# Kernel tuning notes

Hardware: AMD Instinct MI355X
Metric: run time of the kernel (lower is better)

The kernel has to match this reference:

```python
import jax, jax.numpy as jnp
import numpy as np

B = 8
N1, N2 = 65536, 16384
C1, C2 = 256, 512
BN_EPS = 1e-5


def setup_inputs() -> dict:
    key = jax.random.key(0)
    ks = jax.random.split(key, 8)
    xyz1 = jax.random.normal(ks[0], (N1, 3), dtype=jnp.float32)
    points1 = jax.random.normal(ks[1], (N1, C1), dtype=jnp.float32)
    xyz2 = jax.random.normal(ks[2], (N2, 3), dtype=jnp.float32)
    points2 = jax.random.normal(ks[3], (N2, C2), dtype=jnp.float32)
    offset1 = (jnp.arange(1, B + 1, dtype=jnp.int32) * (N1 // B))
    offset2 = (jnp.arange(1, B + 1, dtype=jnp.int32) * (N2 // B))
    W1 = jax.random.normal(ks[4], (C1 + C2, 256), dtype=jnp.float32) * 0.02
    b1 = jnp.zeros((256,), jnp.float32)
    g1 = jnp.ones((256,), jnp.float32)
    be1 = jnp.zeros((256,), jnp.float32)
    W2 = jax.random.normal(ks[5], (256, 256), dtype=jnp.float32) * 0.02
    b2 = jnp.zeros((256,), jnp.float32)
    g2 = jnp.ones((256,), jnp.float32)
    be2 = jnp.zeros((256,), jnp.float32)
    return dict(xyz1=xyz1, points1=points1, xyz2=xyz2, points2=points2,
                offset1=offset1, offset2=offset2,
                W1=W1, b1=b1, g1=g1, be1=be1, W2=W2, b2=b2, g2=g2, be2=be2)


def _knn3(q, k):
    # q: [n1,3] queries, k: [n2,3] reference set -> 3-NN idx + euclidean dist
    d2 = (jnp.sum(q * q, -1)[:, None] + jnp.sum(k * k, -1)[None, :]
          - 2.0 * (q @ k.T))                      # [n1, n2]
    neg_d2, idx = jax.lax.top_k(-d2, 3)           # [n1, 3]
    dist = jnp.sqrt(jnp.maximum(-neg_d2, 0.0))
    return idx, dist


def _bn_relu(x, g, be):
    # BatchNorm1d in training mode: biased batch stats over the point dim
    mu = jnp.mean(x, axis=0)
    var = jnp.mean((x - mu) ** 2, axis=0)
    return jax.nn.relu(g * (x - mu) * jax.lax.rsqrt(var + BN_EPS) + be)


def reference(xyz1, points1, xyz2, points2, offset1, offset2,
              W1, b1, g1, be1, W2, b2, g2, be2):
    bsz = offset1.shape[0]
    n1 = xyz1.shape[0] // bsz
    n2 = xyz2.shape[0] // bsz
    q = xyz1.reshape(bsz, n1, 3)
    k = xyz2.reshape(bsz, n2, 3)
    idx, dist = jax.vmap(_knn3)(q, k)             # [B,n1,3], [B,n1,3]
    gidx = (idx + (jnp.arange(bsz, dtype=idx.dtype) * n2)[:, None, None])
    gidx = gidx.reshape(-1, 3)                    # [N1,3] global row ids
    dist = dist.reshape(-1, 3)
    dist_recip = 1.0 / (dist + 1e-8)
    weight = dist_recip / jnp.sum(dist_recip, axis=1, keepdims=True)
    # fused gather + weighted accumulate: [N1,3,C2] * [N1,3,1] -> [N1,C2]
    interpolated = jnp.sum(points2[gidx] * weight[..., None], axis=1)
    x = jnp.concatenate([points1, interpolated], axis=1)  # [N1, C1+C2]
    x = _bn_relu(x @ W1 + b1, g1, be1)
    x = _bn_relu(x @ W2 + b2, g2, be2)
    return x
```

## Files before the change

### kernel.cpp

```cpp
#include <hip/hip_runtime.h>
#include <math.h>

#define N1T 65536
#define N2T 16384
#define BSZ 8
#define N1B 8192
#define N2B 2048
#define C1 256
#define C2 512
#define K1 768
#define HID 256
#define BN_EPS 1e-5f

typedef short bf16x8 __attribute__((ext_vector_type(8)));
typedef float f32x4 __attribute__((ext_vector_type(4)));

__device__ __forceinline__ float mul_rn(float a, float b) {
    float r; asm("v_mul_f32 %0, %1, %2" : "=v"(r) : "v"(a), "v"(b)); return r;
}
__device__ __forceinline__ float add_rn(float a, float b) {
    float r; asm("v_add_f32 %0, %1, %2" : "=v"(r) : "v"(a), "v"(b)); return r;
}
__device__ __forceinline__ float sub_rn(float a, float b) {
    float r; asm("v_sub_f32 %0, %1, %2" : "=v"(r) : "v"(a), "v"(b)); return r;
}
__device__ __forceinline__ float fma_rn(float a, float b, float c) {
    float r; asm("v_fma_f32 %0, %1, %2, %3" : "=v"(r) : "v"(a), "v"(b), "v"(c)); return r;
}
__device__ __forceinline__ short f2bf(float f) {
    unsigned u = __builtin_bit_cast(unsigned, f);
    u += 0x7fffu + ((u >> 16) & 1u);
    return (short)(u >> 16);
}
__device__ __forceinline__ float bf2f(short s) {
    return __builtin_bit_cast(float, ((unsigned)(unsigned short)s) << 16);
}

__global__ __launch_bounds__(256) void knn_kernel(
    const float* __restrict__ xyz1, const float* __restrict__ xyz2,
    int* __restrict__ idx_out, float* __restrict__ w_out)
{
    __shared__ float4 sref[N2B + 4];
    const int tid = threadIdx.x;
    const int qbase = blockIdx.x * 64;
    const int batch = qbase / N1B;
    const float* k2 = xyz2 + (size_t)batch * N2B * 3;
    for (int p = tid; p < N2B; p += 256) {
        float x = k2[3 * p], y = k2[3 * p + 1], z = k2[3 * p + 2];
        float kk = add_rn(add_rn(mul_rn(x, x), mul_rn(y, y)), mul_rn(z, z));
        sref[p + (p >> 9)] = make_float4(x, y, z, kk);
    }
    __syncthreads();

    const int q = qbase + (tid >> 2);
    const int sub = tid & 3;
    const float qx = xyz1[q * 3 + 0], qy = xyz1[q * 3 + 1], qz = xyz1[q * 3 + 2];
    const float qq = add_rn(add_rn(mul_rn(qx, qx), mul_rn(qy, qy)), mul_rn(qz, qz));

    const int base = sub * 513;
    const int gbase = sub * 512;
    float a0 = 1e30f, a1 = 1e30f, a2 = 1e30f;
    int   ai0 = 0x7fffffff, ai1 = 0x7fffffff, ai2 = 0x7fffffff;
    float c0 = 1e30f, c1 = 1e30f, c2 = 1e30f;
    int   ci0 = 0x7fffffff, ci1 = 0x7fffffff, ci2 = 0x7fffffff;
    for (int jj = 0; jj < 256; ++jj) {
        float4 rA = sref[base + jj];
        float4 rB = sref[base + 256 + jj];
        float pA = mul_rn(qx, rA.x);
        float tA = fma_rn(qz, rA.z, fma_rn(qy, rA.y, pA));
        float dA = add_rn(sub_rn(qq, add_rn(tA, tA)), rA.w);
        float pB = mul_rn(qx, rB.x);
        float tB = fma_rn(qz, rB.z, fma_rn(qy, rB.y, pB));
        float dB = add_rn(sub_rn(qq, add_rn(tB, tB)), rB.w);
        if (dA < a2) {
            if (dA < a1) {
                a2 = a1; ai2 = ai1;
                if (dA < a0) { a1 = a0; ai1 = ai0; a0 = dA; ai0 = gbase + jj; }
                else         { a1 = dA; ai1 = gbase + jj; }
            } else { a2 = dA; ai2 = gbase + jj; }
        }
        if (dB < c2) {
            if (dB < c1) {
                c2 = c1; ci2 = ci1;
                if (dB < c0) { c1 = c0; ci1 = ci0; c0 = dB; ci0 = gbase + 256 + jj; }
                else         { c1 = dB; ci1 = gbase + 256 + jj; }
            } else { c2 = dB; ci2 = gbase + 256 + jj; }
        }
    }
    float bd0 = a0, bd1 = a1, bd2 = a2;
    int   bi0 = ai0, bi1 = ai1, bi2 = ai2;
#define LEXINS(d, ji)                                                        \
    if ((d < bd2) || (d == bd2 && ji < bi2)) {                               \
        if ((d < bd1) || (d == bd1 && ji < bi1)) {                           \
            bd2 = bd1; bi2 = bi1;                                            \
            if ((d < bd0) || (d == bd0 && ji < bi0)) {                       \
                bd1 = bd0; bi1 = bi0; bd0 = d; bi0 = ji;                     \
            } else { bd1 = d; bi1 = ji; }                                    \
        } else { bd2 = d; bi2 = ji; }                                        \
    }
    LEXINS(c0, ci0) LEXINS(c1, ci1) LEXINS(c2, ci2)
#pragma unroll
    for (int mask = 1; mask <= 2; mask <<= 1) {
        float pd0 = __shfl_xor(bd0, mask, 64);
        float pd1 = __shfl_xor(bd1, mask, 64);
        float pd2 = __shfl_xor(bd2, mask, 64);
        int   pi0 = __shfl_xor(bi0, mask, 64);
        int   pi1 = __shfl_xor(bi1, mask, 64);
        int   pi2 = __shfl_xor(bi2, mask, 64);
        LEXINS(pd0, pi0) LEXINS(pd1, pi1) LEXINS(pd2, pi2)
    }
#undef LEXINS
    if (sub == 0) {
        float d0s = __fsqrt_rn(fmaxf(bd0, 0.0f));
        float d1s = __fsqrt_rn(fmaxf(bd1, 0.0f));
        float d2s = __fsqrt_rn(fmaxf(bd2, 0.0f));
        float r0 = __fdiv_rn(1.0f, add_rn(d0s, 1e-8f));
        float r1 = __fdiv_rn(1.0f, add_rn(d1s, 1e-8f));
        float r2 = __fdiv_rn(1.0f, add_rn(d2s, 1e-8f));
        float rs = add_rn(add_rn(r0, r1), r2);
        w_out[q * 3 + 0] = __fdiv_rn(r0, rs);
        w_out[q * 3 + 1] = __fdiv_rn(r1, rs);
        w_out[q * 3 + 2] = __fdiv_rn(r2, rs);
        idx_out[q * 3 + 0] = batch * N2B + bi0;
        idx_out[q * 3 + 1] = batch * N2B + bi1;
        idx_out[q * 3 + 2] = batch * N2B + bi2;
    }
}

__global__ __launch_bounds__(256) void cast_p2_kernel(
    const float* __restrict__ p2, short* __restrict__ p2b)
{
    const size_t i = ((size_t)blockIdx.x * 256 + threadIdx.x) * 8;
    float4 u0 = *(const float4*)(p2 + i);
    float4 u1 = *(const float4*)(p2 + i + 4);
    bf16x8 v;
    v[0] = f2bf(u0.x); v[1] = f2bf(u0.y); v[2] = f2bf(u0.z); v[3] = f2bf(u0.w);
    v[4] = f2bf(u1.x); v[5] = f2bf(u1.y); v[6] = f2bf(u1.z); v[7] = f2bf(u1.w);
    *(bf16x8*)(p2b + i) = v;
}

__global__ __launch_bounds__(256) void transpose_w1_kernel(
    const float* __restrict__ W1, short* __restrict__ w1at, short* __restrict__ w1bt)
{
    const int e = blockIdx.x * 256 + threadIdx.x;
    const int k = e / HID, n = e % HID;
    short v = f2bf(W1[e]);
    if (k < C1) w1at[(size_t)n * C1 + k] = v;
    else        w1bt[(size_t)n * C2 + (k - C1)] = v;
}

__global__ __launch_bounds__(256) void transpose_w_kernel(
    const float* __restrict__ Win, short* __restrict__ WT, int K, int N)
{
    const int e = blockIdx.x * 256 + threadIdx.x;
    const int k = e / N, n = e % N;
    WT[(size_t)n * K + k] = f2bf(Win[e]);
}

#define LDP 40

__global__ __launch_bounds__(256) void zgemm_kernel(
    const short* __restrict__ p2b, const short* __restrict__ w1bt,
    float* __restrict__ Z)
{
    __shared__ short As[128][LDP];
    __shared__ short Bs[128][LDP];
    const int tid = threadIdx.x;
    const int lane = tid & 63, wv = tid >> 6;
    const int wr = wv >> 1, wc = wv & 1;
    const int l16 = lane & 15, kh = (lane >> 4) * 8;
    const int row0 = blockIdx.y * 128, col0 = blockIdx.x * 128;
    f32x4 acc[4][4];
#pragma unroll
    for (int m = 0; m < 4; ++m)
#pragma unroll
        for (int n = 0; n < 4; ++n) acc[m][n] = (f32x4){0.f, 0.f, 0.f, 0.f};

    const int c0 = tid * 2;
    const int r0c = c0 >> 2, kc0 = (c0 & 3) * 8;
    const int r1c = (c0 + 1) >> 2, kc1 = ((c0 + 1) & 3) * 8;

    for (int kt = 0; kt < C2 / 32; ++kt) {
        const int k0 = kt * 32;
        bf16x8 va = *(const bf16x8*)(p2b + (size_t)(row0 + r0c) * C2 + k0 + kc0);
        bf16x8 vb = *(const bf16x8*)(p2b + (size_t)(row0 + r1c) * C2 + k0 + kc1);
        bf16x8 wa = *(const bf16x8*)(w1bt + (size_t)(col0 + r0c) * C2 + k0 + kc0);
        bf16x8 wb = *(const bf16x8*)(w1bt + (size_t)(col0 + r1c) * C2 + k0 + kc1);
        __syncthreads();
        *(bf16x8*)(&As[r0c][kc0]) = va;
        *(bf16x8*)(&As[r1c][kc1]) = vb;
        *(bf16x8*)(&Bs[r0c][kc0]) = wa;
        *(bf16x8*)(&Bs[r1c][kc1]) = wb;
        __syncthreads();

        bf16x8 af[4], bf[4];
#pragma unroll
        for (int m = 0; m < 4; ++m)
            af[m] = *(const bf16x8*)(&As[wr * 64 + m * 16 + l16][kh]);
#pragma unroll
        for (int n = 0; n < 4; ++n)
            bf[n] = *(const bf16x8*)(&Bs[wc * 64 + n * 16 + l16][kh]);
#pragma unroll
        for (int m = 0; m < 4; ++m)
#pragma unroll
            for (int n = 0; n < 4; ++n)
                acc[m][n] = __builtin_amdgcn_mfma_f32_16x16x32_bf16(
                    af[m], bf[n], acc[m][n], 0, 0, 0);
    }
#pragma unroll
    for (int n = 0; n < 4; ++n) {
        const int col = col0 + wc * 64 + n * 16 + l16;
#pragma unroll
        for (int m = 0; m < 4; ++m) {
            const int rowb = row0 + wr * 64 + m * 16 + (lane >> 4) * 4;
#pragma unroll
            for (int j = 0; j < 4; ++j)
                Z[(size_t)(rowb + j) * HID + col] = acc[m][n][j];
        }
    }
}

__global__ __launch_bounds__(512) void gemm1m_kernel(
    const float* __restrict__ points1, const float* __restrict__ Z,
    const int* __restrict__ idx, const float* __restrict__ w,
    const short* __restrict__ w1at, const float* __restrict__ bias,
    short* __restrict__ y1b, float* __restrict__ psum, float* __restrict__ psq)
{
    __shared__ short As[128][LDP];
    __shared__ short Bs[256][LDP];
    __shared__ int   sidx[128][3];
    __shared__ float swt[128][3];
    __shared__ float redS[2][4][64], redQ[2][4][64];
    const int tid = threadIdx.x;
    const int lane = tid & 63, wv = tid >> 6;
    const int wr = wv >> 2, wc = wv & 3;
    const int l16 = lane & 15, kh = (lane >> 4) * 8;
    const int row0 = blockIdx.x * 128;

    if (tid < 128) {
        sidx[tid][0] = idx[(row0 + tid) * 3 + 0];
        sidx[tid][1] = idx[(row0 + tid) * 3 + 1];
        sidx[tid][2] = idx[(row0 + tid) * 3 + 2];
        swt[tid][0] = w[(row0 + tid) * 3 + 0];
        swt[tid][1] = w[(row0 + tid) * 3 + 1];
        swt[tid][2] = w[(row0 + tid) * 3 + 2];
    }

    f32x4 acc[4][4];
#pragma unroll
    for (int m = 0; m < 4; ++m)
#pragma unroll
        for (int n = 0; n < 4; ++n) acc[m][n] = (f32x4){0.f, 0.f, 0.f, 0.f};

    const int arow = tid >> 2, akc = (tid & 3) * 8;
    const int rowA = row0 + arow;
    const int cb0 = tid * 2, cb1 = tid * 2 + 1;
    const int brow0 = cb0 >> 2, bkc0 = (cb0 & 3) * 8;
    const int brow1 = cb1 >> 2, bkc1 = (cb1 & 3) * 8;

#define LOAD_A(VA, KT)                                                        \
    {                                                                         \
        const int k0_ = (KT) * 32;                                            \
        float4 u0 = *(const float4*)(points1 + (size_t)rowA * C1 + k0_ + akc);     \
        float4 u1 = *(const float4*)(points1 + (size_t)rowA * C1 + k0_ + akc + 4); \
        VA[0] = f2bf(u0.x); VA[1] = f2bf(u0.y); VA[2] = f2bf(u0.z); VA[3] = f2bf(u0.w); \
        VA[4] = f2bf(u1.x); VA[5] = f2bf(u1.y); VA[6] = f2bf(u1.z); VA[7] = f2bf(u1.w); \
    }
#define LOAD_B(WA, WB, KT)                                                    \
    {                                                                         \
        const int k0_ = (KT) * 32;                                            \
        WA = *(const bf16x8*)(w1at + (size_t)brow0 * C1 + k0_ + bkc0);        \
        WB = *(const bf16x8*)(w1at + (size_t)brow1 * C1 + k0_ + bkc1);        \
    }

    bf16x8 va, wa, wb;
    LOAD_A(va, 0)
    LOAD_B(wa, wb, 0)
    for (int kt = 0; kt < C1 / 32; ++kt) {
        __syncthreads();
        *(bf16x8*)(&As[arow][akc]) = va;
        *(bf16x8*)(&Bs[brow0][bkc0]) = wa;
        *(bf16x8*)(&Bs[brow1][bkc1]) = wb;
        __syncthreads();
        if (kt + 1 < C1 / 32) {
            LOAD_A(va, kt + 1)
            LOAD_B(wa, wb, kt + 1)
        }
        bf16x8 af[4], bf[4];
#pragma unroll
        for (int m = 0; m < 4; ++m)
            af[m] = *(const bf16x8*)(&As[wr * 64 + m * 16 + l16][kh]);
#pragma unroll
        for (int n = 0; n < 4; ++n)
            bf[n] = *(const bf16x8*)(&Bs[wc * 64 + n * 16 + l16][kh]);
#pragma unroll
        for (int m = 0; m < 4; ++m)
#pragma unroll
            for (int n = 0; n < 4; ++n)
                acc[m][n] = __builtin_amdgcn_mfma_f32_16x16x32_bf16(
                    af[m], bf[n], acc[m][n], 0, 0, 0);
    }
#undef LOAD_A
#undef LOAD_B
    float bv[4];
#pragma unroll
    for (int n = 0; n < 4; ++n) bv[n] = bias[wc * 64 + n * 16 + l16];
    float s[4] = {0.f, 0.f, 0.f, 0.f}, qa[4] = {0.f, 0.f, 0.f, 0.f};
#pragma unroll
    for (int m = 0; m < 4; ++m) {
        const int rl0 = wr * 64 + m * 16 + (lane >> 4) * 4;
#pragma unroll
        for (int j = 0; j < 4; ++j) {
            const int rl = rl0 + j;
            const int j0 = sidx[rl][0], j1 = sidx[rl][1], j2 = sidx[rl][2];
            const float w0 = swt[rl][0], w1 = swt[rl][1], w2 = swt[rl][2];
            const float* z0 = Z + (size_t)j0 * HID;
            const float* z1 = Z + (size_t)j1 * HID;
            const float* z2 = Z + (size_t)j2 * HID;
#pragma unroll
            for (int n = 0; n < 4; ++n) {
                const int col = wc * 64 + n * 16 + l16;
                float zi = fmaf(w0, z0[col], fmaf(w1, z1[col], w2 * z2[col]));
                float v = acc[m][n][j] + bv[n] + zi;
                y1b[(size_t)(row0 + rl) * HID + col] = f2bf(v);
                s[n] += v; qa[n] = fmaf(v, v, qa[n]);
            }
        }
    }
#pragma unroll
    for (int n = 0; n < 4; ++n) {
        float sv = s[n], qv = qa[n];
        sv += __shfl_xor(sv, 16, 64);  sv += __shfl_xor(sv, 32, 64);
        qv += __shfl_xor(qv, 16, 64);  qv += __shfl_xor(qv, 32, 64);
        if ((lane >> 4) == 0) {
            redS[wr][wc][n * 16 + l16] = sv;
            redQ[wr][wc][n * 16 + l16] = qv;
        }
    }
    __syncthreads();
    if (tid < 256) {
        const int wcf = tid >> 6, cf = tid & 63;
        float sv = redS[0][wcf][cf] + redS[1][wcf][cf];
        float qv = redQ[0][wcf][cf] + redQ[1][wcf][cf];
        psum[(size_t)blockIdx.x * HID + tid] = sv;
        psq[(size_t)blockIdx.x * HID + tid] = qv;
    }
}

#define GEMM_EPILOGUE(STORE_STMT)                                             \
    __shared__ float redS[2][2][64], redQ[2][2][64];                          \
    _Pragma("unroll")                                                         \
    for (int n = 0; n < 4; ++n) {                                             \
        const int col = col0 + wc * 64 + n * 16 + l16;                        \
        const float bv = bias[col];                                           \
        float s = 0.f, qa = 0.f;                                              \
        _Pragma("unroll")                                                     \
        for (int m = 0; m < 4; ++m) {                                         \
            const int rowb = row0 + wr * 64 + m * 16 + (lane >> 4) * 4;       \
            _Pragma("unroll")                                                 \
            for (int j = 0; j < 4; ++j) {                                     \
                float v = acc[m][n][j] + bv;                                  \
                STORE_STMT;                                                   \
                s += v; qa = fmaf(v, v, qa);                                  \
            }                                                                 \
        }                                                                     \
        s += __shfl_xor(s, 16, 64);  s += __shfl_xor(s, 32, 64);              \
        qa += __shfl_xor(qa, 16, 64); qa += __shfl_xor(qa, 32, 64);           \
        if ((lane >> 4) == 0) {                                               \
            redS[wr][wc][n * 16 + l16] = s;                                   \
            redQ[wr][wc][n * 16 + l16] = qa;                                  \
        }                                                                     \
    }                                                                         \
    __syncthreads();                                                          \
    if (tid < 128) {                                                          \
        const int wcf = tid >> 6, cf = tid & 63;                              \
        float s = redS[0][wcf][cf] + redS[1][wcf][cf];                        \
        float qa = redQ[0][wcf][cf] + redQ[1][wcf][cf];                       \
        const int gcol = col0 + wcf * 64 + cf;                                \
        psum[(size_t)blockIdx.y * HID + gcol] = s;                            \
        psq[(size_t)blockIdx.y * HID + gcol] = qa;                            \
    }

__global__ __launch_bounds__(256) void gemm2m_kernel(
    const short* __restrict__ y1b, const float* __restrict__ scale,
    const float* __restrict__ shift, const short* __restrict__ w2t,
    const float* __restrict__ bias, short* __restrict__ y2b,
    float* __restrict__ psum, float* __restrict__ psq)
{
    __shared__ short As[128][LDP];
    __shared__ short Bs[128][LDP];
    const int tid = threadIdx.x;
    const int lane = tid & 63, wv = tid >> 6;
    const int wr = wv >> 1, wc = wv & 1;
    const int l16 = lane & 15, kh = (lane >> 4) * 8;
    const int row0 = blockIdx.y * 128, col0 = blockIdx.x * 128;
    f32x4 acc[4][4];
#pragma unroll
    for (int m = 0; m < 4; ++m)
#pragma unroll
        for (int n = 0; n < 4; ++n) acc[m][n] = (f32x4){0.f, 0.f, 0.f, 0.f};

    const int c0 = tid * 2;
    const int r0c = c0 >> 2, kc0 = (c0 & 3) * 8;
    const int r1c = (c0 + 1) >> 2, kc1 = ((c0 + 1) & 3) * 8;

    for (int kt = 0; kt < HID / 32; ++kt) {
        const int k0 = kt * 32;
        bf16x8 x0 = *(const bf16x8*)(y1b + (size_t)(row0 + r0c) * HID + k0 + kc0);
        bf16x8 x1 = *(const bf16x8*)(y1b + (size_t)(row0 + r1c) * HID + k0 + kc1);
        float4 s0 = *(const float4*)(scale + k0 + kc0);
        float4 s1 = *(const float4*)(scale + k0 + kc0 + 4);
        float4 h0 = *(const float4*)(shift + k0 + kc0);
        float4 h1 = *(const float4*)(shift + k0 + kc0 + 4);
        float4 s2 = *(const float4*)(scale + k0 + kc1);
        float4 s3 = *(const float4*)(scale + k0 + kc1 + 4);
        float4 h2 = *(const float4*)(shift + k0 + kc1);
        float4 h3 = *(const float4*)(shift + k0 + kc1 + 4);
        bf16x8 va, vb;
        va[0] = f2bf(fmaxf(fmaf(bf2f(x0[0]), s0.x, h0.x), 0.f));
        va[1] = f2bf(fmaxf(fmaf(bf2f(x0[1]), s0.y, h0.y), 0.f));
        va[2] = f2bf(fmaxf(fmaf(bf2f(x0[2]), s0.z, h0.z), 0.f));
        va[3] = f2bf(fmaxf(fmaf(bf2f(x0[3]), s0.w, h0.w), 0.f));
        va[4] = f2bf(fmaxf(fmaf(bf2f(x0[4]), s1.x, h1.x), 0.f));
        va[5] = f2bf(fmaxf(fmaf(bf2f(x0[5]), s1.y, h1.y), 0.f));
        va[6] = f2bf(fmaxf(fmaf(bf2f(x0[6]), s1.z, h1.z), 0.f));
        va[7] = f2bf(fmaxf(fmaf(bf2f(x0[7]), s1.w, h1.w), 0.f));
        vb[0] = f2bf(fmaxf(fmaf(bf2f(x1[0]), s2.x, h2.x), 0.f));
        vb[1] = f2bf(fmaxf(fmaf(bf2f(x1[1]), s2.y, h2.y), 0.f));
        vb[2] = f2bf(fmaxf(fmaf(bf2f(x1[2]), s2.z, h2.z), 0.f));
        vb[3] = f2bf(fmaxf(fmaf(bf2f(x1[3]), s2.w, h2.w), 0.f));
        vb[4] = f2bf(fmaxf(fmaf(bf2f(x1[4]), s3.x, h3.x), 0.f));
        vb[5] = f2bf(fmaxf(fmaf(bf2f(x1[5]), s3.y, h3.y), 0.f));
        vb[6] = f2bf(fmaxf(fmaf(bf2f(x1[6]), s3.z, h3.z), 0.f));
        vb[7] = f2bf(fmaxf(fmaf(bf2f(x1[7]), s3.w, h3.w), 0.f));
        bf16x8 wa = *(const bf16x8*)(w2t + (size_t)(col0 + r0c) * HID + k0 + kc0);
        bf16x8 wb = *(const bf16x8*)(w2t + (size_t)(col0 + r1c) * HID + k0 + kc1);
        __syncthreads();
        *(bf16x8*)(&As[r0c][kc0]) = va;
        *(bf16x8*)(&As[r1c][kc1]) = vb;
        *(bf16x8*)(&Bs[r0c][kc0]) = wa;
        *(bf16x8*)(&Bs[r1c][kc1]) = wb;
        __syncthreads();

        bf16x8 af[4], bf[4];
#pragma unroll
        for (int m = 0; m < 4; ++m)
            af[m] = *(const bf16x8*)(&As[wr * 64 + m * 16 + l16][kh]);
#pragma unroll
        for (int n = 0; n < 4; ++n)
            bf[n] = *(const bf16x8*)(&Bs[wc * 64 + n * 16 + l16][kh]);
#pragma unroll
        for (int m = 0; m < 4; ++m)
#pragma unroll
            for (int n = 0; n < 4; ++n)
                acc[m][n] = __builtin_amdgcn_mfma_f32_16x16x32_bf16(
                    af[m], bf[n], acc[m][n], 0, 0, 0);
    }
    GEMM_EPILOGUE(y2b[(size_t)(rowb + j) * HID + col] = f2bf(v))
}

__global__ __launch_bounds__(256) void bn_finalize_kernel(
    const float* __restrict__ psum, const float* __restrict__ psq,
    const float* __restrict__ g, const float* __restrict__ be,
    float* __restrict__ scale, float* __restrict__ shift)
{
    const int c = threadIdx.x;
    float s = 0.0f, q = 0.0f;
    for (int b = 0; b < 512; ++b) { s += psum[b * HID + c]; q += psq[b * HID + c]; }
    const float inv_n = 1.0f / (float)N1T;
    const float mu = s * inv_n;
    const float var = fmaxf(q * inv_n - mu * mu, 0.0f);
    const float sc = g[c] * rsqrtf(var + BN_EPS);
    scale[c] = sc;
    shift[c] = be[c] - mu * sc;
}

__global__ __launch_bounds__(256) void bn_apply_kernel(
    const short* __restrict__ y2b, const float* __restrict__ scale,
    const float* __restrict__ shift, float* __restrict__ out)
{
    const size_t i = ((size_t)blockIdx.x * 256 + threadIdx.x) * 8;
    const int c8 = (int)(i & 255);
    bf16x8 x = *(const bf16x8*)(y2b + i);
    float4 s0 = *(const float4*)(scale + c8);
    float4 s1 = *(const float4*)(scale + c8 + 4);
    float4 h0 = *(const float4*)(shift + c8);
    float4 h1 = *(const float4*)(shift + c8 + 4);
    float4 o0, o1;
    o0.x = fmaxf(fmaf(bf2f(x[0]), s0.x, h0.x), 0.f);
    o0.y = fmaxf(fmaf(bf2f(x[1]), s0.y, h0.y), 0.f);
    o0.z = fmaxf(fmaf(bf2f(x[2]), s0.z, h0.z), 0.f);
    o0.w = fmaxf(fmaf(bf2f(x[3]), s0.w, h0.w), 0.f);
    o1.x = fmaxf(fmaf(bf2f(x[4]), s1.x, h1.x), 0.f);
    o1.y = fmaxf(fmaf(bf2f(x[5]), s1.y, h1.y), 0.f);
    o1.z = fmaxf(fmaf(bf2f(x[6]), s1.z, h1.z), 0.f);
    o1.w = fmaxf(fmaf(bf2f(x[7]), s1.w, h1.w), 0.f);
    *(float4*)(out + i) = o0;
    *(float4*)(out + i + 4) = o1;
}

extern "C" void kernel_launch(void* const* d_in, const int* in_sizes, int n_in,
                              void* d_out, int out_size, void* d_ws, size_t ws_size,
                              hipStream_t stream)
{
    const float* xyz1    = (const float*)d_in[0];
    const float* points1 = (const float*)d_in[1];
    const float* xyz2    = (const float*)d_in[2];
    const float* points2 = (const float*)d_in[3];
    const float* W1  = (const float*)d_in[6];
    const float* b1  = (const float*)d_in[7];
    const float* g1  = (const float*)d_in[8];
    const float* be1 = (const float*)d_in[9];
    const float* W2  = (const float*)d_in[10];
    const float* b2  = (const float*)d_in[11];
    const float* g2  = (const float*)d_in[12];
    const float* be2 = (const float*)d_in[13];
    float* out = (float*)d_out;

    char* ws = (char*)d_ws;
    short* y1b  = (short*)ws;
    short* y2b  = (short*)(ws + 33554432);
    short* p2b  = (short*)(ws + 67108864);
    float* Z    = (float*)(ws + 67108864 + 16777216);
    size_t off  = 67108864 + 16777216 + 16777216;
    short*  w1at   = (short*)(ws + off);  off += (size_t)C1 * HID * 2;
    short*  w1bt   = (short*)(ws + off);  off += (size_t)C2 * HID * 2;
    short*  w2t    = (short*)(ws + off);  off += (size_t)HID * HID * 2;
    int*    idx    = (int*)(ws + off);    off += (size_t)N1T * 3 * 4;
    float*  w      = (float*)(ws + off);  off += (size_t)N1T * 3 * 4;
    float*  psum   = (float*)(ws + off);  off += 512 * 256 * 4;
    float*  psq    = (float*)(ws + off);  off += 512 * 256 * 4;
    float*  scale1 = (float*)(ws + off);  off += 256 * 4;
    float*  shift1 = (float*)(ws + off);  off += 256 * 4;
    float*  scale2 = (float*)(ws + off);  off += 256 * 4;
    float*  shift2 = (float*)(ws + off);  off += 256 * 4;

    cast_p2_kernel<<<N2T * C2 / 8 / 256, 256, 0, stream>>>(points2, p2b);
    transpose_w1_kernel<<<K1 * HID / 256, 256, 0, stream>>>(W1, w1at, w1bt);
    transpose_w_kernel<<<HID * HID / 256, 256, 0, stream>>>(W2, w2t, HID, HID);
    zgemm_kernel<<<dim3(HID / 128, N2T / 128), 256, 0, stream>>>(p2b, w1bt, Z);
    knn_kernel<<<1024, 256, 0, stream>>>(xyz1, xyz2, idx, w);
    gemm1m_kernel<<<N1T / 128, 512, 0, stream>>>(
        points1, Z, idx, w, w1at, b1, y1b, psum, psq);
    bn_finalize_kernel<<<1, 256, 0, stream>>>(psum, psq, g1, be1, scale1, shift1);
    gemm2m_kernel<<<dim3(HID / 128, N1T / 128), 256, 0, stream>>>(
        y1b, scale1, shift1, w2t, b2, y2b, psum, psq);
    bn_finalize_kernel<<<1, 256, 0, stream>>>(psum, psq, g2, be2, scale2, shift2);
    bn_apply_kernel<<<N1T * HID / 8 / 256, 256, 0, stream>>>(y2b, scale2, shift2, out);
}
```

Before: 233.8 us.

## Fuse points2 cast into Z GEMM and co-schedule it with kNN

Drops the standalone points2 bf16 cast kernel. The Z GEMM now reads fp32 points2 and converts it to bf16 on the fly while staging tiles into shared memory. The Z GEMM and the kNN search are merged into one launch, split by block index, so the two independent workloads can run concurrently. The two weight-transpose kernels are also merged into one launch. This removes several launches and the write and read of a 16 MB intermediate, at the cost of more global read bytes per GEMM tile, conversion work inside the GEMM loop, and a shared-memory size sized for the larger kNN branch.

```diff
diff --git a/kernel.cpp b/kernel.cpp
--- a/kernel.cpp
+++ b/kernel.cpp
@@ -36,13 +36,104 @@
     return __builtin_bit_cast(float, ((unsigned)(unsigned short)s) << 16);
 }
 
-__global__ __launch_bounds__(256) void knn_kernel(
+#define LDP 40
+
+__global__ __launch_bounds__(256) void prep_w_kernel(
+    const float* __restrict__ W1, const float* __restrict__ W2,
+    short* __restrict__ w1at, short* __restrict__ w1bt, short* __restrict__ w2t)
+{
+    const int bid = blockIdx.x;
+    if (bid < 768) {
+        const int e = bid * 256 + threadIdx.x;
+        const int k = e / HID, n = e % HID;
+        short v = f2bf(W1[e]);
+        if (k < C1) w1at[(size_t)n * C1 + k] = v;
+        else        w1bt[(size_t)n * C2 + (k - C1)] = v;
+    } else {
+        const int e = (bid - 768) * 256 + threadIdx.x;
+        const int k = e / HID, n = e % HID;
+        w2t[(size_t)n * HID + k] = f2bf(W2[e]);
+    }
+}
+
+__global__ __launch_bounds__(256) void phase1_kernel(
+    const float* __restrict__ points2, const short* __restrict__ w1bt,
+    float* __restrict__ Z,
     const float* __restrict__ xyz1, const float* __restrict__ xyz2,
     int* __restrict__ idx_out, float* __restrict__ w_out)
 {
-    __shared__ float4 sref[N2B + 4];
+    __shared__ __align__(16) char smem[32832];
+    const int bid = blockIdx.x;
     const int tid = threadIdx.x;
-    const int qbase = blockIdx.x * 64;
+
+    if (bid < 256) {
+        short (*As)[LDP] = (short(*)[LDP])smem;
+        short (*Bs)[LDP] = (short(*)[LDP])(smem + 128 * LDP * 2);
+        const int lane = tid & 63, wv = tid >> 6;
+        const int wr = wv >> 1, wc = wv & 1;
+        const int l16 = lane & 15, kh = (lane >> 4) * 8;
+        const int row0 = (bid >> 1) * 128, col0 = (bid & 1) * 128;
+        f32x4 acc[4][4];
+#pragma unroll
+        for (int m = 0; m < 4; ++m)
+#pragma unroll
+            for (int n = 0; n < 4; ++n) acc[m][n] = (f32x4){0.f, 0.f, 0.f, 0.f};
+
+        const int c0 = tid * 2;
+        const int r0c = c0 >> 2, kc0 = (c0 & 3) * 8;
+        const int r1c = (c0 + 1) >> 2, kc1 = ((c0 + 1) & 3) * 8;
+
+        for (int kt = 0; kt < C2 / 32; ++kt) {
+            const int k0 = kt * 32;
+            float4 u0 = *(const float4*)(points2 + (size_t)(row0 + r0c) * C2 + k0 + kc0);
+            float4 u1 = *(const float4*)(points2 + (size_t)(row0 + r0c) * C2 + k0 + kc0 + 4);
+            float4 u2 = *(const float4*)(points2 + (size_t)(row0 + r1c) * C2 + k0 + kc1);
+            float4 u3 = *(const float4*)(points2 + (size_t)(row0 + r1c) * C2 + k0 + kc1 + 4);
+            bf16x8 va, vb;
+            va[0] = f2bf(u0.x); va[1] = f2bf(u0.y); va[2] = f2bf(u0.z); va[3] = f2bf(u0.w);
+            va[4] = f2bf(u1.x); va[5] = f2bf(u1.y); va[6] = f2bf(u1.z); va[7] = f2bf(u1.w);
+            vb[0] = f2bf(u2.x); vb[1] = f2bf(u2.y); vb[2] = f2bf(u2.z); vb[3] = f2bf(u2.w);
+            vb[4] = f2bf(u3.x); vb[5] = f2bf(u3.y); vb[6] = f2bf(u3.z); vb[7] = f2bf(u3.w);
+            bf16x8 wa = *(const bf16x8*)(w1bt + (size_t)(col0 + r0c) * C2 + k0 + kc0);
+            bf16x8 wb = *(const bf16x8*)(w1bt + (size_t)(col0 + r1c) * C2 + k0 + kc1);
+            __syncthreads();
+            *(bf16x8*)(&As[r0c][kc0]) = va;
+            *(bf16x8*)(&As[r1c][kc1]) = vb;
+            *(bf16x8*)(&Bs[r0c][kc0]) = wa;
+            *(bf16x8*)(&Bs[r1c][kc1]) = wb;
+            __syncthreads();
+
+            bf16x8 af[4], bf[4];
+#pragma unroll
+            for (int m = 0; m < 4; ++m)
+                af[m] = *(const bf16x8*)(&As[wr * 64 + m * 16 + l16][kh]);
+#pragma unroll
+            for (int n = 0; n < 4; ++n)
+                bf[n] = *(const bf16x8*)(&Bs[wc * 64 + n * 16 + l16][kh]);
+#pragma unroll
+            for (int m = 0; m < 4; ++m)
+#pragma unroll
+                for (int n = 0; n < 4; ++n)
+                    acc[m][n] = __builtin_amdgcn_mfma_f32_16x16x32_bf16(
+                        af[m], bf[n], acc[m][n], 0, 0, 0);
+        }
+#pragma unroll
+        for (int n = 0; n < 4; ++n) {
+            const int col = col0 + wc * 64 + n * 16 + l16;
+#pragma unroll
+            for (int m = 0; m < 4; ++m) {
+                const int rowb = row0 + wr * 64 + m * 16 + (lane >> 4) * 4;
+#pragma unroll
+                for (int j = 0; j < 4; ++j)
+                    Z[(size_t)(rowb + j) * HID + col] = acc[m][n][j];
+            }
+        }
+        return;
+    }
+
+    float4* sref = (float4*)smem;
+    const int kb = bid - 256;
+    const int qbase = kb * 64;
     const int batch = qbase / N1B;
     const float* k2 = xyz2 + (size_t)batch * N2B * 3;
     for (int p = tid; p < N2B; p += 256) {
@@ -124,99 +215,6 @@
         idx_out[q * 3 + 0] = batch * N2B + bi0;
         idx_out[q * 3 + 1] = batch * N2B + bi1;
         idx_out[q * 3 + 2] = batch * N2B + bi2;
-    }
-}
-
-__global__ __launch_bounds__(256) void cast_p2_kernel(
-    const float* __restrict__ p2, short* __restrict__ p2b)
-{
-    const size_t i = ((size_t)blockIdx.x * 256 + threadIdx.x) * 8;
-    float4 u0 = *(const float4*)(p2 + i);
-    float4 u1 = *(const float4*)(p2 + i + 4);
-    bf16x8 v;
-    v[0] = f2bf(u0.x); v[1] = f2bf(u0.y); v[2] = f2bf(u0.z); v[3] = f2bf(u0.w);
-    v[4] = f2bf(u1.x); v[5] = f2bf(u1.y); v[6] = f2bf(u1.z); v[7] = f2bf(u1.w);
-    *(bf16x8*)(p2b + i) = v;
-}
-
-__global__ __launch_bounds__(256) void transpose_w1_kernel(
-    const float* __restrict__ W1, short* __restrict__ w1at, short* __restrict__ w1bt)
-{
-    const int e = blockIdx.x * 256 + threadIdx.x;
-    const int k = e / HID, n = e % HID;
-    short v = f2bf(W1[e]);
-    if (k < C1) w1at[(size_t)n * C1 + k] = v;
-    else        w1bt[(size_t)n * C2 + (k - C1)] = v;
-}
-
-__global__ __launch_bounds__(256) void transpose_w_kernel(
-    const float* __restrict__ Win, short* __restrict__ WT, int K, int N)
-{
-    const int e = blockIdx.x * 256 + threadIdx.x;
-    const int k = e / N, n = e % N;
-    WT[(size_t)n * K + k] = f2bf(Win[e]);
-}
-
-#define LDP 40
-
-__global__ __launch_bounds__(256) void zgemm_kernel(
-    const short* __restrict__ p2b, const short* __restrict__ w1bt,
-    float* __restrict__ Z)
-{
-    __shared__ short As[128][LDP];
-    __shared__ short Bs[128][LDP];
-    const int tid = threadIdx.x;
-    const int lane = tid & 63, wv = tid >> 6;
-    const int wr = wv >> 1, wc = wv & 1;
-    const int l16 = lane & 15, kh = (lane >> 4) * 8;
-    const int row0 = blockIdx.y * 128, col0 = blockIdx.x * 128;
-    f32x4 acc[4][4];
-#pragma unroll
-    for (int m = 0; m < 4; ++m)
-#pragma unroll
-        for (int n = 0; n < 4; ++n) acc[m][n] = (f32x4){0.f, 0.f, 0.f, 0.f};
-
-    const int c0 = tid * 2;
-    const int r0c = c0 >> 2, kc0 = (c0 & 3) * 8;
-    const int r1c = (c0 + 1) >> 2, kc1 = ((c0 + 1) & 3) * 8;
-
-    for (int kt = 0; kt < C2 / 32; ++kt) {
-        const int k0 = kt * 32;
-        bf16x8 va = *(const bf16x8*)(p2b + (size_t)(row0 + r0c) * C2 + k0 + kc0);
-        bf16x8 vb = *(const bf16x8*)(p2b + (size_t)(row0 + r1c) * C2 + k0 + kc1);
-        bf16x8 wa = *(const bf16x8*)(w1bt + (size_t)(col0 + r0c) * C2 + k0 + kc0);
-        bf16x8 wb = *(const bf16x8*)(w1bt + (size_t)(col0 + r1c) * C2 + k0 + kc1);
-        __syncthreads();
-        *(bf16x8*)(&As[r0c][kc0]) = va;
-        *(bf16x8*)(&As[r1c][kc1]) = vb;
-        *(bf16x8*)(&Bs[r0c][kc0]) = wa;
-        *(bf16x8*)(&Bs[r1c][kc1]) = wb;
-        __syncthreads();
-
-        bf16x8 af[4], bf[4];
-#pragma unroll
-        for (int m = 0; m < 4; ++m)
-            af[m] = *(const bf16x8*)(&As[wr * 64 + m * 16 + l16][kh]);
-#pragma unroll
-        for (int n = 0; n < 4; ++n)
-            bf[n] = *(const bf16x8*)(&Bs[wc * 64 + n * 16 + l16][kh]);
-#pragma unroll
-        for (int m = 0; m < 4; ++m)
-#pragma unroll
-            for (int n = 0; n < 4; ++n)
-                acc[m][n] = __builtin_amdgcn_mfma_f32_16x16x32_bf16(
-                    af[m], bf[n], acc[m][n], 0, 0, 0);
-    }
-#pragma unroll
-    for (int n = 0; n < 4; ++n) {
-        const int col = col0 + wc * 64 + n * 16 + l16;
-#pragma unroll
-        for (int m = 0; m < 4; ++m) {
-            const int rowb = row0 + wr * 64 + m * 16 + (lane >> 4) * 4;
-#pragma unroll
-            for (int j = 0; j < 4; ++j)
-                Z[(size_t)(rowb + j) * HID + col] = acc[m][n][j];
-        }
     }
 }
 
@@ -520,9 +518,8 @@
     char* ws = (char*)d_ws;
     short* y1b  = (short*)ws;
     short* y2b  = (short*)(ws + 33554432);
-    short* p2b  = (short*)(ws + 67108864);
-    float* Z    = (float*)(ws + 67108864 + 16777216);
-    size_t off  = 67108864 + 16777216 + 16777216;
+    float* Z    = (float*)(ws + 67108864);
+    size_t off  = 67108864 + 16777216;
     short*  w1at   = (short*)(ws + off);  off += (size_t)C1 * HID * 2;
     short*  w1bt   = (short*)(ws + off);  off += (size_t)C2 * HID * 2;
     short*  w2t    = (short*)(ws + off);  off += (size_t)HID * HID * 2;
@@ -535,11 +532,9 @@
     float*  scale2 = (float*)(ws + off);  off += 256 * 4;
     float*  shift2 = (float*)(ws + off);  off += 256 * 4;
 
-    cast_p2_kernel<<<N2T * C2 / 8 / 256, 256, 0, stream>>>(points2, p2b);
-    transpose_w1_kernel<<<K1 * HID / 256, 256, 0, stream>>>(W1, w1at, w1bt);
-    transpose_w_kernel<<<HID * HID / 256, 256, 0, stream>>>(W2, w2t, HID, HID);
-    zgemm_kernel<<<dim3(HID / 128, N2T / 128), 256, 0, stream>>>(p2b, w1bt, Z);
-    knn_kernel<<<1024, 256, 0, stream>>>(xyz1, xyz2, idx, w);
+    prep_w_kernel<<<1024, 256, 0, stream>>>(W1, W2, w1at, w1bt, w2t);
+    phase1_kernel<<<1280, 256, 0, stream>>>(points2, w1bt, Z,
+                                            xyz1, xyz2, idx, w);
     gemm1m_kernel<<<N1T / 128, 512, 0, stream>>>(
         points1, Z, idx, w, w1at, b1, y1b, psum, psq);
     bn_finalize_kernel<<<1, 256, 0, stream>>>(psum, psq, g1, be1, scale1, shift1);
```

After: 230.5 us. About the same (-1.4%).
